# Kernel tuning notes

Measured on AMD Instinct MI355X. Metric: run time of the kernel, lower is better.

The kernel has to match this reference:

```python
import jax, jax.numpy as jnp
import numpy as np
import math

NUM_HEADS = 12
HEAD_DIM = 64
DEGREE = 3
POLY_DIM = HEAD_DIM * (DEGREE + 1)  # 256
MEM_HID = 512
HIDDEN = 768


def setup_inputs() -> dict:
    key = jax.random.key(0)
    ks = jax.random.split(key, 6)
    B, S = 4, 2048
    hidden_states = jax.random.normal(ks[0], (B, S, HIDDEN), dtype=jnp.float32)
    # q projection weight stored (in, out) so y = x @ Wq
    Wq = jax.random.normal(ks[1], (HIDDEN, HIDDEN), dtype=jnp.float32) / np.sqrt(HIDDEN)
    # polynomial coefficients initialized to 1/i!
    coeffs = jnp.array([1.0 / math.factorial(i) for i in range(DEGREE + 1)], dtype=jnp.float32)
    # deep memory MLP: Linear(poly_dim->mem_hid) + ReLU + Linear(mem_hid->poly_dim)
    W1 = jax.random.normal(ks[2], (POLY_DIM, MEM_HID), dtype=jnp.float32) / np.sqrt(POLY_DIM)
    b1 = jnp.zeros((MEM_HID,), dtype=jnp.float32)
    W2 = jax.random.normal(ks[3], (MEM_HID, POLY_DIM), dtype=jnp.float32) / np.sqrt(MEM_HID)
    b2 = jnp.zeros((POLY_DIM,), dtype=jnp.float32)
    return {"hidden_states": hidden_states, "Wq": Wq, "coeffs": coeffs,
            "W1": W1, "b1": b1, "W2": W2, "b2": b2}


def _poly_map(x, coeffs):
    # x: [..., head_dim] -> [..., head_dim*(degree+1)]
    xs = jnp.clip(x, -10.0, 10.0)
    feats = [coeffs[0] * jnp.ones_like(x)]
    for i in range(1, DEGREE + 1):
        feats.append(jnp.clip(coeffs[i] * xs ** i, -1e6, 1e6))
    return jnp.concatenate(feats, axis=-1)


def reference(hidden_states, Wq, coeffs, W1, b1, W2, b2):
    B, S, H = hidden_states.shape
    # q projection -> [B, S, nh, hd]
    q = (hidden_states @ Wq).reshape(B, S, NUM_HEADS, HEAD_DIM)
    # polynomial feature expansion -> [B, S, nh, poly_dim]
    poly_q = _poly_map(q, coeffs)
    flat = poly_q.reshape(-1, POLY_DIM)  # [B*S*nh, poly_dim]
    # deep memory MLP (test-time memory read)
    h = jax.nn.relu(flat @ W1 + b1)
    mem = h @ W2 + b2  # [B*S*nh, poly_dim]
    # slice first head_dim dims, fold heads back into hidden
    out = mem[:, :HEAD_DIM].reshape(B, S, NUM_HEADS * HEAD_DIM)
    return out
```

## Files before the change

kernel.cpp:

```cpp
#include <hip/hip_runtime.h>


typedef unsigned short u16;
typedef __attribute__((ext_vector_type(8))) short short8;
typedef __attribute__((ext_vector_type(4))) float f32x4;
typedef __attribute__((ext_vector_type(4))) u16 u16x4;

__device__ __forceinline__ u16 f2bf(float f) {
    unsigned u = __builtin_bit_cast(unsigned, f);
    u += 0x7FFFu + ((u >> 16) & 1u);
    return (u16)(u >> 16);
}

__device__ __forceinline__ unsigned cvtpk_bf16(float lo, float hi) {
    unsigned r;
    asm("v_cvt_pk_bf16_f32 %0, %1, %2" : "=v"(r) : "v"(lo), "v"(hi));
    return r;
}

__device__ __forceinline__ void gl2lds16(const void* g, void* l) {
    __builtin_amdgcn_global_load_lds(
        (const __attribute__((address_space(1))) unsigned int*)g,
        (__attribute__((address_space(3))) unsigned int*)l, 16, 0, 0);
}


__global__ __launch_bounds__(256)
void prep(const float* __restrict__ X, u16* __restrict__ Xb,
          const float* __restrict__ Wq, u16* __restrict__ Wqb,
          const float* __restrict__ W1, u16* __restrict__ W1b,
          const float* __restrict__ W2, u16* __restrict__ W2b,
          const float* __restrict__ b1, const float* __restrict__ coeffs,
          float* __restrict__ b1e)
{
    __shared__ float t[32][33];
    const int b = blockIdx.x, tid = threadIdx.x;

    if (b < 6144) {
        const int i = b * 256 + tid;
        float4 v = reinterpret_cast<const float4*>(X)[i];
        u16x4 o = {f2bf(v.x), f2bf(v.y), f2bf(v.z), f2bf(v.w)};
        reinterpret_cast<u16x4*>(Xb)[i] = o;
    } else if (b < 6880) {
        const float* in; u16* out; int R, Cin, bx, by;
        int lb = b - 6144;
        if (lb < 576)      { in = Wq; out = Wqb; R = 768; Cin = 768; bx = lb % 24; by = lb / 24; }
        else if (lb < 704) { lb -= 576; in = W1; out = W1b; R = 256; Cin = 512; bx = lb % 16; by = lb / 16; }
        else               { lb -= 704; in = W2; out = W2b; R = 512; Cin = 256; bx = lb % 2;  by = lb / 2; }
        const int c0 = bx * 32, r0 = by * 32;
        const int tx = tid & 31, ty = tid >> 5;
        #pragma unroll
        for (int j = 0; j < 32; j += 8)
            t[ty + j][tx] = in[(size_t)(r0 + ty + j) * Cin + c0 + tx];
        __syncthreads();
        #pragma unroll
        for (int j = 0; j < 32; j += 8)
            out[(size_t)(c0 + ty + j) * R + r0 + tx] = f2bf(t[tx][ty + j]);
    } else {
        const int n = (b - 6880) * 256 + tid;
        float s = 0.f;
        #pragma unroll 8
        for (int k = 0; k < 64; ++k) s += W1[k * 512 + n];
        b1e[n] = b1[n] + coeffs[0] * s;
    }
}


__global__ __launch_bounds__(256)
void gemm1_poly(const u16* __restrict__ Xb, const u16* __restrict__ Wqb,
                const float* __restrict__ coeffs, u16* __restrict__ P)
{
    __shared__ u16 lds[128 * 200];

    const int tid = threadIdx.x;
    const int w = tid >> 6, lane = tid & 63;
    const int lrow = lane >> 2, lslot = lane & 3;
    const int m16 = lane & 15, quad = lane >> 4;
    const int w0 = w & 1, w1 = w >> 1;
    const int tok0 = blockIdx.x * 64;
    const int bn = blockIdx.y * 128;
    const int h0 = blockIdx.y * 2;

    const float c1 = coeffs[1], c2 = coeffs[2], c3 = coeffs[3];

    f32x4 acc[4][2];
    #pragma unroll
    for (int i = 0; i < 4; ++i)
        #pragma unroll
        for (int j = 0; j < 2; ++j)
            acc[i][j] = (f32x4){0.f, 0.f, 0.f, 0.f};

    auto stage = [&](int buf, int k0) {
        u16* Xs = lds + buf * 6144;
        u16* Ws = Xs + 2048;
        {
            const int row = w * 16 + lrow;
            const int cc = lslot ^ ((row >> 2) & 3);
            gl2lds16(Xb + (size_t)(tok0 + row) * 768 + k0 + cc * 8, &Xs[row * 32 + lslot * 8]);
        }
        #pragma unroll
        for (int i = 0; i < 2; ++i) {
            const int row = (w * 2 + i) * 16 + lrow;
            const int cc = lslot ^ ((row >> 2) & 3);
            gl2lds16(Wqb + (size_t)(bn + row) * 768 + k0 + cc * 8, &Ws[row * 32 + lslot * 8]);
        }
    };

    stage(0, 0);
    __syncthreads();
    int cur = 0;

    for (int k0 = 0; k0 < 768; k0 += 32) {
        if (k0 + 32 < 768) stage(cur ^ 1, k0 + 32);
        const u16* Xs = lds + cur * 6144;
        const u16* Ws = Xs + 2048;
        short8 a[4], b[2];
        #pragma unroll
        for (int i = 0; i < 4; ++i) {
            const int row = w0 * 64 + i * 16 + m16;
            const int ss = quad ^ ((row >> 2) & 3);
            a[i] = *reinterpret_cast<const short8*>(&Ws[row * 32 + ss * 8]);
        }
        #pragma unroll
        for (int j = 0; j < 2; ++j) {
            const int row = w1 * 32 + j * 16 + m16;
            const int ss = quad ^ ((row >> 2) & 3);
            b[j] = *reinterpret_cast<const short8*>(&Xs[row * 32 + ss * 8]);
        }
        #pragma unroll
        for (int i = 0; i < 4; ++i)
            #pragma unroll
            for (int j = 0; j < 2; ++j)
                acc[i][j] = __builtin_amdgcn_mfma_f32_16x16x32_bf16(a[i], b[j], acc[i][j], 0, 0, 0);
        __syncthreads();
        cur ^= 1;
    }

    #pragma unroll
    for (int i = 0; i < 4; ++i) {
        const int d0 = i * 16 + quad * 4;
        #pragma unroll
        for (int j = 0; j < 2; ++j) {
            const int tokLocal = w1 * 32 + j * 16 + m16;
            u16* base = &lds[(tokLocal * 2 + w0) * 200 + d0];
            float x[4], x2[4];
            #pragma unroll
            for (int r = 0; r < 4; ++r) {
                x[r] = fminf(fmaxf(acc[i][j][r], -10.f), 10.f);
                x2[r] = x[r] * x[r];
            }
            uint2 p1, p2, p3;
            p1.x = cvtpk_bf16(c1 * x[0], c1 * x[1]);
            p1.y = cvtpk_bf16(c1 * x[2], c1 * x[3]);
            p2.x = cvtpk_bf16(c2 * x2[0], c2 * x2[1]);
            p2.y = cvtpk_bf16(c2 * x2[2], c2 * x2[3]);
            p3.x = cvtpk_bf16(c3 * x2[0] * x[0], c3 * x2[1] * x[1]);
            p3.y = cvtpk_bf16(c3 * x2[2] * x[2], c3 * x2[3] * x[3]);
            *reinterpret_cast<uint2*>(base)       = p1;
            *reinterpret_cast<uint2*>(base + 64)  = p2;
            *reinterpret_cast<uint2*>(base + 128) = p3;
        }
    }
    __syncthreads();

    #pragma unroll
    for (int ii = 0; ii < 12; ++ii) {
        const int flat = ii * 256 + tid;
        const int rowL = flat / 24, ck = flat % 24;
        const int tokL = rowL >> 1, hh = rowL & 1;
        const size_t prow = ((size_t)(tok0 + tokL) * 12 + h0 + hh);
        short8 v = *reinterpret_cast<const short8*>(&lds[rowL * 200 + ck * 8]);
        *reinterpret_cast<short8*>(P + prow * 192 + ck * 8) = v;
    }
}

__global__ __launch_bounds__(256)
void gemm23(const u16* __restrict__ P, const u16* __restrict__ W1t,
            const float* __restrict__ b1e, const u16* __restrict__ W2t,
            const float* __restrict__ b2, float* __restrict__ out)
{
    __shared__ u16 As[128 * 32];
    __shared__ u16 Bs[128 * 32];
    __shared__ u16 Hs[4][128 * 32];

    const int tid = threadIdx.x;
    const int w = tid >> 6, lane = tid & 63;
    const int lrow = lane >> 2, lslot = lane & 3;
    const int m16 = lane & 15, quad = lane >> 4;
    const size_t r0 = (size_t)blockIdx.x * 128;
    const int w0 = w & 1, w1 = w >> 1;

    f32x4 accO[4][2];
    #pragma unroll
    for (int i = 0; i < 4; ++i)
        #pragma unroll
        for (int j = 0; j < 2; ++j)
            accO[i][j] = (f32x4){0.f, 0.f, 0.f, 0.f};

    #pragma unroll 1
    for (int s = 0; s < 4; ++s) {
        f32x4 accH[4][4];
        #pragma unroll
        for (int i = 0; i < 4; ++i)
            #pragma unroll
            for (int j = 0; j < 4; ++j)
                accH[i][j] = (f32x4){0.f, 0.f, 0.f, 0.f};

        for (int c = 0; c < 6; ++c) {
            #pragma unroll
            for (int i = 0; i < 2; ++i) {
                const int row = (w * 2 + i) * 16 + lrow;
                const int cc = lslot ^ ((row >> 2) & 3);
                gl2lds16(W1t + (size_t)(s * 128 + row) * 256 + 64 + c * 32 + cc * 8,
                         &As[row * 32 + lslot * 8]);
                gl2lds16(P + (r0 + row) * 192 + c * 32 + cc * 8,
                         &Bs[row * 32 + lslot * 8]);
            }
            __syncthreads();

            short8 af[4], bf[4];
            #pragma unroll
            for (int i = 0; i < 4; ++i) {
                const int row = w0 * 64 + i * 16 + m16;
                const int ss = quad ^ ((row >> 2) & 3);
                af[i] = *reinterpret_cast<const short8*>(&As[row * 32 + ss * 8]);
            }
            #pragma unroll
            for (int j = 0; j < 4; ++j) {
                const int row = w1 * 64 + j * 16 + m16;
                const int ss = quad ^ ((row >> 2) & 3);
                bf[j] = *reinterpret_cast<const short8*>(&Bs[row * 32 + ss * 8]);
            }
            #pragma unroll
            for (int i = 0; i < 4; ++i)
                #pragma unroll
                for (int j = 0; j < 4; ++j)
                    accH[i][j] = __builtin_amdgcn_mfma_f32_16x16x32_bf16(af[i], bf[j], accH[i][j], 0, 0, 0);
            __syncthreads();
        }

        #pragma unroll
        for (int i = 0; i < 4; ++i) {
            const int lb = w0 * 64 + i * 16 + quad * 4;
            const f32x4 bv = *reinterpret_cast<const f32x4*>(&b1e[s * 128 + lb]);
            const int hc = lb >> 5;
            #pragma unroll
            for (int j = 0; j < 4; ++j) {
                const int tc = w1 * 64 + j * 16 + m16;
                const float h0 = fmaxf(accH[i][j][0] + bv[0], 0.f);
                const float h1 = fmaxf(accH[i][j][1] + bv[1], 0.f);
                const float h2 = fmaxf(accH[i][j][2] + bv[2], 0.f);
                const float h3 = fmaxf(accH[i][j][3] + bv[3], 0.f);
                uint2 v;
                v.x = cvtpk_bf16(h0, h1);
                v.y = cvtpk_bf16(h2, h3);
                const int sl = ((lb >> 3) & 3) ^ ((tc >> 2) & 3);
                *reinterpret_cast<uint2*>(&Hs[hc][tc * 32 + sl * 8 + (lb & 7)]) = v;
            }
        }

        {
            u16* dst = (w < 2) ? As : Bs;
            #pragma unroll
            for (int i = 0; i < 4; ++i) {
                const int row = i * 16 + lrow;
                const int cc = lslot ^ ((row >> 2) & 3);
                gl2lds16(W2t + (size_t)row * 512 + s * 128 + w * 32 + cc * 8,
                         dst + (w & 1) * 2048 + row * 32 + lslot * 8);
            }
        }
        __syncthreads();

        #pragma unroll
        for (int c = 0; c < 4; ++c) {
            short8 a3[4], b3[2];
            #pragma unroll
            for (int i = 0; i < 4; ++i) {
                const int tr = w0 * 64 + i * 16 + m16;
                const int ss = quad ^ ((tr >> 2) & 3);
                a3[i] = *reinterpret_cast<const short8*>(&Hs[c][tr * 32 + ss * 8]);
            }
            const u16* wsrc = ((c < 2) ? (const u16*)As : (const u16*)Bs) + (c & 1) * 2048;
            #pragma unroll
            for (int j = 0; j < 2; ++j) {
                const int rowb = w1 * 32 + j * 16 + m16;
                const int ss = quad ^ ((rowb >> 2) & 3);
                b3[j] = *reinterpret_cast<const short8*>(wsrc + rowb * 32 + ss * 8);
            }
            #pragma unroll
            for (int i = 0; i < 4; ++i)
                #pragma unroll
                for (int j = 0; j < 2; ++j)
                    accO[i][j] = __builtin_amdgcn_mfma_f32_16x16x32_bf16(a3[i], b3[j], accO[i][j], 0, 0, 0);
        }
        __syncthreads();
    }

    #pragma unroll
    for (int j = 0; j < 2; ++j) {
        const int col = w1 * 32 + j * 16 + m16;
        const float bv = b2[col];
        #pragma unroll
        for (int i = 0; i < 4; ++i) {
            #pragma unroll
            for (int r = 0; r < 4; ++r) {
                const int row = w0 * 64 + i * 16 + quad * 4 + r;
                out[(r0 + row) * 64 + col] = accO[i][j][r] + bv;
            }
        }
    }
}


extern "C" void kernel_launch(void* const* d_in, const int* in_sizes, int n_in,
                              void* d_out, int out_size, void* d_ws, size_t ws_size,
                              hipStream_t stream) {
    const float* X      = (const float*)d_in[0];
    const float* Wq     = (const float*)d_in[1];
    const float* coeffs = (const float*)d_in[2];
    const float* W1     = (const float*)d_in[3];
    const float* b1     = (const float*)d_in[4];
    const float* W2     = (const float*)d_in[5];
    const float* b2     = (const float*)d_in[6];

    char* ws = (char*)d_ws;
    u16*   Xb  = (u16*)(ws);
    u16*   Wqb = (u16*)(ws + 12582912);
    u16*   W1b = (u16*)(ws + 13762560);
    u16*   W2b = (u16*)(ws + 14024704);
    float* b1e = (float*)(ws + 14090240);
    u16*   P   = (u16*)(ws + 14092288);

    prep<<<6882, 256, 0, stream>>>(X, Xb, Wq, Wqb, W1, W1b, W2, W2b, b1, coeffs, b1e);

    gemm1_poly<<<dim3(128, 6), 256, 0, stream>>>(Xb, Wqb, coeffs, P);

    gemm23<<<dim3(768), 256, 0, stream>>>(P, W1b, b1e, W2b, b2, (float*)d_out);
}
```

Baseline: 163.3 us.

## Triple-buffer GEMM staging with manual waitcnt barriers and register-held W2

Both GEMM kernels move from double buffering with __syncthreads to a three-slot LDS ring. Hand-written s_waitcnt vmcnt/lgkmcnt plus s_barrier let two global-to-LDS loads stay in flight while MFMA work runs on the current slot. In gemm23 the W2 tiles are now loaded straight from global memory into registers instead of going through LDS, which removes a barrier-bound staging step. Launch bounds are also raised to request higher occupancy. The hand-counted vmcnt values are fragile, and an off-by-one count or clamped redundant load could race or waste bandwidth.

```diff
diff --git a/kernel.cpp b/kernel.cpp
--- a/kernel.cpp
+++ b/kernel.cpp
@@ -23,6 +23,11 @@
         (const __attribute__((address_space(1))) unsigned int*)g,
         (__attribute__((address_space(3))) unsigned int*)l, 16, 0, 0);
 }
+
+#define WAIT_VM_LGKM_BAR(N) \
+    asm volatile("s_waitcnt vmcnt(" #N ") lgkmcnt(0)\n\ts_barrier" ::: "memory")
+#define WAIT_LGKM_BAR() \
+    asm volatile("s_waitcnt lgkmcnt(0)\n\ts_barrier" ::: "memory")
 
 
 __global__ __launch_bounds__(256)
@@ -66,7 +71,7 @@
 }
 
 
-__global__ __launch_bounds__(256)
+__global__ __launch_bounds__(256, 3)
 void gemm1_poly(const u16* __restrict__ Xb, const u16* __restrict__ Wqb,
                 const float* __restrict__ coeffs, u16* __restrict__ P)
 {
@@ -90,8 +95,9 @@
         for (int j = 0; j < 2; ++j)
             acc[i][j] = (f32x4){0.f, 0.f, 0.f, 0.f};
 
-    auto stage = [&](int buf, int k0) {
-        u16* Xs = lds + buf * 6144;
+    auto stage = [&](int slot, int g) {
+        const int k0 = g * 32;
+        u16* Xs = lds + slot * 6144;
         u16* Ws = Xs + 2048;
         {
             const int row = w * 16 + lrow;
@@ -107,12 +113,14 @@
     };
 
     stage(0, 0);
-    __syncthreads();
-    int cur = 0;
-
-    for (int k0 = 0; k0 < 768; k0 += 32) {
-        if (k0 + 32 < 768) stage(cur ^ 1, k0 + 32);
-        const u16* Xs = lds + cur * 6144;
+    stage(1, 1);
+
+    #pragma unroll 1
+    for (int g = 0; g < 24; ++g) {
+        WAIT_VM_LGKM_BAR(3);
+        const int gg = (g + 2 <= 23) ? g + 2 : 23;
+        stage((g + 2) % 3, gg);
+        const u16* Xs = lds + (g % 3) * 6144;
         const u16* Ws = Xs + 2048;
         short8 a[4], b[2];
         #pragma unroll
@@ -132,9 +140,9 @@
             #pragma unroll
             for (int j = 0; j < 2; ++j)
                 acc[i][j] = __builtin_amdgcn_mfma_f32_16x16x32_bf16(a[i], b[j], acc[i][j], 0, 0, 0);
-        __syncthreads();
-        cur ^= 1;
-    }
+    }
+
+    asm volatile("s_waitcnt vmcnt(0) lgkmcnt(0)\n\ts_barrier" ::: "memory");
 
     #pragma unroll
     for (int i = 0; i < 4; ++i) {
@@ -174,13 +182,13 @@
     }
 }
 
-__global__ __launch_bounds__(256)
+
+__global__ __launch_bounds__(256, 2)
 void gemm23(const u16* __restrict__ P, const u16* __restrict__ W1t,
             const float* __restrict__ b1e, const u16* __restrict__ W2t,
             const float* __restrict__ b2, float* __restrict__ out)
 {
-    __shared__ u16 As[128 * 32];
-    __shared__ u16 Bs[128 * 32];
+    __shared__ u16 ring[3][8192];
     __shared__ u16 Hs[4][128 * 32];
 
     const int tid = threadIdx.x;
@@ -190,12 +198,44 @@
     const size_t r0 = (size_t)blockIdx.x * 128;
     const int w0 = w & 1, w1 = w >> 1;
 
+    auto stageTo = [&](int slot, int g) {
+        const int s = g / 6, c = g % 6;
+        u16* W1s = ring[slot];
+        u16* Ps  = ring[slot] + 4096;
+        #pragma unroll
+        for (int i = 0; i < 2; ++i) {
+            const int row = (w * 2 + i) * 16 + lrow;
+            const int cc = lslot ^ ((row >> 2) & 3);
+            gl2lds16(W1t + (size_t)(s * 128 + row) * 256 + 64 + c * 32 + cc * 8,
+                     &W1s[row * 32 + lslot * 8]);
+            gl2lds16(P + (r0 + row) * 192 + c * 32 + cc * 8,
+                     &Ps[row * 32 + lslot * 8]);
+        }
+    };
+    auto stageClamped = [&](int slot, int gg) {
+        if (gg <= 23) stageTo(slot, gg);
+        else if (gg == 24) stageTo(slot, 23);
+    };
+
+    short8 b3s[4][2];
+    auto loadW2 = [&](int s) {
+        #pragma unroll
+        for (int c = 0; c < 4; ++c)
+            #pragma unroll
+            for (int j = 0; j < 2; ++j)
+                b3s[c][j] = *reinterpret_cast<const short8*>(
+                    W2t + (size_t)(w1 * 32 + j * 16 + m16) * 512 + s * 128 + c * 32 + quad * 8);
+    };
+
     f32x4 accO[4][2];
     #pragma unroll
     for (int i = 0; i < 4; ++i)
         #pragma unroll
         for (int j = 0; j < 2; ++j)
             accO[i][j] = (f32x4){0.f, 0.f, 0.f, 0.f};
+
+    stageTo(0, 0);
+    stageTo(1, 1);
 
     #pragma unroll 1
     for (int s = 0; s < 4; ++s) {
@@ -206,38 +246,36 @@
             for (int j = 0; j < 4; ++j)
                 accH[i][j] = (f32x4){0.f, 0.f, 0.f, 0.f};
 
-        for (int c = 0; c < 6; ++c) {
-            #pragma unroll
-            for (int i = 0; i < 2; ++i) {
-                const int row = (w * 2 + i) * 16 + lrow;
-                const int cc = lslot ^ ((row >> 2) & 3);
-                gl2lds16(W1t + (size_t)(s * 128 + row) * 256 + 64 + c * 32 + cc * 8,
-                         &As[row * 32 + lslot * 8]);
-                gl2lds16(P + (r0 + row) * 192 + c * 32 + cc * 8,
-                         &Bs[row * 32 + lslot * 8]);
-            }
-            __syncthreads();
-
+        auto computeH = [&](int slot) {
+            const u16* W1s = ring[slot];
+            const u16* Ps  = ring[slot] + 4096;
             short8 af[4], bf[4];
             #pragma unroll
             for (int i = 0; i < 4; ++i) {
                 const int row = w0 * 64 + i * 16 + m16;
                 const int ss = quad ^ ((row >> 2) & 3);
-                af[i] = *reinterpret_cast<const short8*>(&As[row * 32 + ss * 8]);
+                af[i] = *reinterpret_cast<const short8*>(&W1s[row * 32 + ss * 8]);
             }
             #pragma unroll
             for (int j = 0; j < 4; ++j) {
                 const int row = w1 * 64 + j * 16 + m16;
                 const int ss = quad ^ ((row >> 2) & 3);
-                bf[j] = *reinterpret_cast<const short8*>(&Bs[row * 32 + ss * 8]);
+                bf[j] = *reinterpret_cast<const short8*>(&Ps[row * 32 + ss * 8]);
             }
             #pragma unroll
             for (int i = 0; i < 4; ++i)
                 #pragma unroll
                 for (int j = 0; j < 4; ++j)
                     accH[i][j] = __builtin_amdgcn_mfma_f32_16x16x32_bf16(af[i], bf[j], accH[i][j], 0, 0, 0);
-            __syncthreads();
-        }
+        };
+
+        const int g0 = s * 6;
+        WAIT_VM_LGKM_BAR(4);  stageClamped(2, g0 + 2); loadW2(s); computeH(0);
+        WAIT_VM_LGKM_BAR(12); stageClamped(0, g0 + 3);            computeH(1);
+        WAIT_VM_LGKM_BAR(4);  stageClamped(1, g0 + 4);            computeH(2);
+        WAIT_VM_LGKM_BAR(4);  stageClamped(2, g0 + 5);            computeH(0);
+        WAIT_VM_LGKM_BAR(4);  stageClamped(0, g0 + 6);            computeH(1);
+        WAIT_VM_LGKM_BAR(4);  stageClamped(1, g0 + 7);            computeH(2);
 
         #pragma unroll
         for (int i = 0; i < 4; ++i) {
@@ -259,42 +297,26 @@
             }
         }
 
-        {
-            u16* dst = (w < 2) ? As : Bs;
-            #pragma unroll
-            for (int i = 0; i < 4; ++i) {
-                const int row = i * 16 + lrow;
-                const int cc = lslot ^ ((row >> 2) & 3);
-                gl2lds16(W2t + (size_t)row * 512 + s * 128 + w * 32 + cc * 8,
-                         dst + (w & 1) * 2048 + row * 32 + lslot * 8);
-            }
-        }
-        __syncthreads();
+        WAIT_LGKM_BAR();
 
         #pragma unroll
         for (int c = 0; c < 4; ++c) {
-            short8 a3[4], b3[2];
+            short8 a3[4];
             #pragma unroll
             for (int i = 0; i < 4; ++i) {
                 const int tr = w0 * 64 + i * 16 + m16;
                 const int ss = quad ^ ((tr >> 2) & 3);
                 a3[i] = *reinterpret_cast<const short8*>(&Hs[c][tr * 32 + ss * 8]);
             }
-            const u16* wsrc = ((c < 2) ? (const u16*)As : (const u16*)Bs) + (c & 1) * 2048;
-            #pragma unroll
-            for (int j = 0; j < 2; ++j) {
-                const int rowb = w1 * 32 + j * 16 + m16;
-                const int ss = quad ^ ((rowb >> 2) & 3);
-                b3[j] = *reinterpret_cast<const short8*>(wsrc + rowb * 32 + ss * 8);
-            }
             #pragma unroll
             for (int i = 0; i < 4; ++i)
                 #pragma unroll
                 for (int j = 0; j < 2; ++j)
-                    accO[i][j] = __builtin_amdgcn_mfma_f32_16x16x32_bf16(a3[i], b3[j], accO[i][j], 0, 0, 0);
-        }
-        __syncthreads();
-    }
+                    accO[i][j] = __builtin_amdgcn_mfma_f32_16x16x32_bf16(a3[i], b3s[c][j], accO[i][j], 0, 0, 0);
+        }
+    }
+
+    asm volatile("s_waitcnt vmcnt(0)" ::: "memory");
 
     #pragma unroll
     for (int j = 0; j < 2; ++j) {
```

Measured after the change: 166.2 us. About the same (+1.8%).
